# Optimization experiments

Measured on AMD Instinct MI355X. Metric: run time of the kernel, lower is better.

## Reference

```python
import jax, jax.numpy as jnp
import numpy as np

B, LQ, LKV, D, H = 4, 1024, 4096, 512, 4
HD = D // H  # head dim = 128


def setup_inputs() -> dict:
    key = jax.random.key(0)
    ks = jax.random.split(key, 6)
    s = 1.0 / np.sqrt(D)
    return {
        "x": jax.random.normal(ks[0], (B, LQ, D), jnp.float32),
        "encoder_feats": jax.random.normal(ks[1], (B, LKV, D), jnp.float32),
        "Wq": jax.random.normal(ks[2], (D, D), jnp.float32) * s,
        "Wk": jax.random.normal(ks[3], (D, D), jnp.float32) * s,
        "Wv": jax.random.normal(ks[4], (D, D), jnp.float32) * s,
        "bq": jnp.zeros((D,), jnp.float32),
        "bk": jnp.zeros((D,), jnp.float32),
        "bv": jnp.zeros((D,), jnp.float32),
        "Wo": jax.random.normal(ks[5], (D, D), jnp.float32) * s,
        "bo": jnp.zeros((D,), jnp.float32),
    }


def reference(x, encoder_feats, Wq, Wk, Wv, bq, bk, bv, Wo, bo):
    # nn.MultiheadAttention explicit (non-flash) path, dropout=0, eval.
    # Project, split heads: [B, L, D] -> [B, H, L, HD]
    def heads(t, L):
        return t.reshape(B, L, H, HD).transpose(0, 2, 1, 3)

    q = heads(x @ Wq.T + bq, LQ)
    k = heads(encoder_feats @ Wk.T + bk, LKV)
    v = heads(encoder_feats @ Wv.T + bv, LKV)

    scale = 1.0 / jnp.sqrt(jnp.asarray(HD, x.dtype))
    scores = jnp.einsum("bhqd,bhkd->bhqk", q, k) * scale  # [B,H,LQ,LKV]
    attn = jax.nn.softmax(scores, axis=-1)
    ctx = jnp.einsum("bhqk,bhkd->bhqd", attn, v)  # [B,H,LQ,HD]
    ctx = ctx.transpose(0, 2, 1, 3).reshape(B, LQ, D)
    attn_output = ctx @ Wo.T + bo
    # forward() returns attn_output only (fused/LayerNorm result is discarded)
    return attn_output
```

## Files before the change

kernel.cpp:

```cpp
#include <hip/hip_runtime.h>
#include <math.h>

#define B_    4
#define LQ_   1024
#define LKV_  4096
#define DM    512
#define NH    4
#define HD_   128

typedef _Float16 half8   __attribute__((ext_vector_type(8)));
typedef _Float16 half4_t __attribute__((ext_vector_type(4)));
typedef float    floatx4 __attribute__((ext_vector_type(4)));

#define MFMA16(a, b, c) __builtin_amdgcn_mfma_f32_16x16x32_f16((a), (b), (c), 0, 0, 0)

template<typename XT, int MODE>
__global__ __launch_bounds__(256) void proj_mfma(
    const XT* __restrict__ X,
    const float* __restrict__ W,
    const float* __restrict__ bias,
    void* __restrict__ Yv, float scale)
{
  __shared__ _Float16 SMEM[128 * 144];
  _Float16 (*Xs)[72] = (_Float16(*)[72])SMEM;
  _Float16 (*Ws)[72] = (_Float16(*)[72])(SMEM + 128 * 72);

  const int tid  = threadIdx.x;
  const int lane = tid & 63;
  const int w    = tid >> 6;
  const int n16  = lane & 15;
  const int quad = lane >> 4;
  const int wm   = (w & 1) * 64;
  const int wn   = (w >> 1) * 64;
  const int row0 = blockIdx.x * 128;
  const int col0 = blockIdx.y * 128;

  floatx4 acc[4][4];
#pragma unroll
  for (int a = 0; a < 4; ++a)
#pragma unroll
    for (int b = 0; b < 4; ++b) acc[a][b] = (floatx4){0.f, 0.f, 0.f, 0.f};

  for (int k0 = 0; k0 < 512; k0 += 64) {
#pragma unroll
    for (int i = 0; i < 4; ++i) {
      int c = i * 256 + tid;
      int r = c >> 3, off = (c & 7) * 8;
      half8 hx;
      if (sizeof(XT) == 4) {
        const float* xp = (const float*)X + (size_t)(row0 + r) * 512 + k0 + off;
        float4 a = *(const float4*)xp, b2 = *(const float4*)(xp + 4);
        hx[0] = (_Float16)a.x;  hx[1] = (_Float16)a.y;
        hx[2] = (_Float16)a.z;  hx[3] = (_Float16)a.w;
        hx[4] = (_Float16)b2.x; hx[5] = (_Float16)b2.y;
        hx[6] = (_Float16)b2.z; hx[7] = (_Float16)b2.w;
      } else {
        hx = *(const half8*)((const _Float16*)X + (size_t)(row0 + r) * 512 + k0 + off);
      }
      *(half8*)&Xs[r][off] = hx;
      const float* wp = W + (size_t)(col0 + r) * 512 + k0 + off;
      float4 wa = *(const float4*)wp, wb = *(const float4*)(wp + 4);
      half8 hw;
      hw[0] = (_Float16)wa.x; hw[1] = (_Float16)wa.y;
      hw[2] = (_Float16)wa.z; hw[3] = (_Float16)wa.w;
      hw[4] = (_Float16)wb.x; hw[5] = (_Float16)wb.y;
      hw[6] = (_Float16)wb.z; hw[7] = (_Float16)wb.w;
      *(half8*)&Ws[r][off] = hw;
    }
    __syncthreads();
#pragma unroll
    for (int kc = 0; kc < 2; ++kc) {
      half8 af[4], bf[4];
#pragma unroll
      for (int mb = 0; mb < 4; ++mb)
        af[mb] = *(const half8*)&Xs[wm + mb * 16 + n16][kc * 32 + quad * 8];
#pragma unroll
      for (int nb = 0; nb < 4; ++nb)
        bf[nb] = *(const half8*)&Ws[wn + nb * 16 + n16][kc * 32 + quad * 8];
#pragma unroll
      for (int mb = 0; mb < 4; ++mb)
#pragma unroll
        for (int nb = 0; nb < 4; ++nb)
          acc[mb][nb] = MFMA16(af[mb], bf[nb], acc[mb][nb]);
    }
    __syncthreads();
  }

  if (MODE == 2) {
    _Float16 (*Ts)[144] = (_Float16(*)[144])SMEM;
#pragma unroll
    for (int mb = 0; mb < 4; ++mb) {
#pragma unroll
      for (int nb = 0; nb < 4; ++nb) {
        int dl = wn + nb * 16 + n16;
        float bi = bias[col0 + dl];
        half4_t hv;
#pragma unroll
        for (int r = 0; r < 4; ++r) hv[r] = (_Float16)(acc[mb][nb][r] + bi);
        *(half4_t*)&Ts[dl][wm + mb * 16 + quad * 4] = hv;
      }
    }
    __syncthreads();
    int b   = row0 >> 12;
    int kv0 = row0 & 4095;
    _Float16* Vt = (_Float16*)Yv;
#pragma unroll
    for (int i = 0; i < 8; ++i) {
      int f = i * 256 + tid;
      int dl = f >> 4, kv8 = (f & 15) * 8;
      half8 ov = *(const half8*)&Ts[dl][kv8];
      *(half8*)(Vt + (size_t)((b * 4 + blockIdx.y) * 128 + dl) * LKV_ + kv0 + kv8) = ov;
    }
  } else {
#pragma unroll
    for (int mb = 0; mb < 4; ++mb) {
#pragma unroll
      for (int nb = 0; nb < 4; ++nb) {
#pragma unroll
        for (int r = 0; r < 4; ++r) {
          int row = row0 + wm + mb * 16 + quad * 4 + r;
          int col = col0 + wn + nb * 16 + n16;
          float v = (acc[mb][nb][r] + bias[col]) * scale;
          if (MODE == 0) ((float*)Yv)[(size_t)row * 512 + col] = v;
          else ((_Float16*)Yv)[(size_t)row * 512 + col] = (_Float16)v;
        }
      }
    }
  }
}

__global__ __launch_bounds__(256, 2) void flash_mfma2(
    const _Float16* __restrict__ Qh,
    const _Float16* __restrict__ Kh,
    const _Float16* __restrict__ Vtg,
    _Float16* __restrict__ Opart,
    float* __restrict__ ml)
{
  __shared__ _Float16 Ks[64][136];
  __shared__ _Float16 Vs[128][72];
  __shared__ _Float16 Ps[4][32][72];

  const int tid  = threadIdx.x;
  const int lane = tid & 63;
  const int w    = tid >> 6;
  const int n16  = lane & 15;
  const int quad = lane >> 4;

  const int xb    = blockIdx.x;
  const int qt    = blockIdx.y;
  const int split = xb & 3;
  const int bh    = xb >> 2;
  const int h = bh & 3, b = bh >> 2;

  const _Float16* Qg = Qh + (size_t)(b * LQ_ + qt * 128) * DM + h * HD_;
  const _Float16* Kg = Kh + (size_t)(b * LKV_) * DM + h * HD_;
  const _Float16* Vg = Vtg + (size_t)(bh * HD_) * LKV_;

  half8 qf[2][4];
  const int chunk = w >> 1;
  const int qrb   = (w & 1) * 32;
#pragma unroll
  for (int c = 0; c < 2; ++c) {
#pragma unroll
    for (int i = 0; i < 4; ++i) {
      int f = i * 256 + tid;
      int r = f >> 4, c8 = (f & 15) * 8;
      *(half8*)&Ks[r][c8] = *(const half8*)(Qg + (size_t)(c * 64 + r) * DM + c8);
    }
    __syncthreads();
    if (chunk == c) {
#pragma unroll
      for (int qb = 0; qb < 2; ++qb)
#pragma unroll
        for (int kc = 0; kc < 4; ++kc)
          qf[qb][kc] = *(const half8*)&Ks[qrb + qb * 16 + n16][kc * 32 + quad * 8];
    }
    __syncthreads();
  }

  floatx4 o[2][8];
#pragma unroll
  for (int mb = 0; mb < 2; ++mb)
#pragma unroll
    for (int vb = 0; vb < 8; ++vb) o[mb][vb] = (floatx4){0.f, 0.f, 0.f, 0.f};
  float m_i[2] = {-INFINITY, -INFINITY};
  float l_i[2] = {0.f, 0.f};

  for (int kt = split * 16; kt < split * 16 + 16; ++kt) {
#pragma unroll
    for (int i = 0; i < 4; ++i) {
      int f = i * 256 + tid;
      int r = f >> 4, c8 = (f & 15) * 8;
      *(half8*)&Ks[r][c8] = *(const half8*)(Kg + (size_t)(kt * 64 + r) * DM + c8);
    }
#pragma unroll
    for (int i = 0; i < 4; ++i) {
      int f = i * 256 + tid;
      int d = f >> 3, kv8 = (f & 7) * 8;
      *(half8*)&Vs[d][kv8] = *(const half8*)(Vg + (size_t)d * LKV_ + kt * 64 + kv8);
    }
    __syncthreads();

    floatx4 s[2][4];
#pragma unroll
    for (int qb = 0; qb < 2; ++qb)
#pragma unroll
      for (int cb = 0; cb < 4; ++cb) s[qb][cb] = (floatx4){0.f, 0.f, 0.f, 0.f};
#pragma unroll
    for (int cb = 0; cb < 4; ++cb) {
#pragma unroll
      for (int kc = 0; kc < 4; ++kc) {
        half8 kf = *(const half8*)&Ks[cb * 16 + n16][kc * 32 + quad * 8];
        s[0][cb] = MFMA16(kf, qf[0][kc], s[0][cb]);
        s[1][cb] = MFMA16(kf, qf[1][kc], s[1][cb]);
      }
    }

    float alpha[2];
#pragma unroll
    for (int qb = 0; qb < 2; ++qb) {
      float mx = -INFINITY;
#pragma unroll
      for (int cb = 0; cb < 4; ++cb)
#pragma unroll
        for (int r = 0; r < 4; ++r) mx = fmaxf(mx, s[qb][cb][r]);
      mx = fmaxf(mx, __shfl_xor(mx, 16));
      mx = fmaxf(mx, __shfl_xor(mx, 32));
      float mn = fmaxf(m_i[qb], mx);
      alpha[qb] = __expf(m_i[qb] - mn);
      m_i[qb] = mn;
      float rs = 0.f;
#pragma unroll
      for (int cb = 0; cb < 4; ++cb) {
        half4_t ph;
#pragma unroll
        for (int r = 0; r < 4; ++r) {
          float p = __expf(s[qb][cb][r] - mn);
          rs += p;
          ph[r] = (_Float16)p;
        }
        *(half4_t*)&Ps[w][qb * 16 + n16][cb * 16 + quad * 4] = ph;
      }
      rs += __shfl_xor(rs, 16);
      rs += __shfl_xor(rs, 32);
      l_i[qb] = l_i[qb] * alpha[qb] + rs;
    }

#pragma unroll
    for (int mb = 0; mb < 2; ++mb) {
#pragma unroll
      for (int r = 0; r < 4; ++r) {
        float a = __shfl(alpha[mb], (lane & 48) | (quad * 4 + r));
#pragma unroll
        for (int vb = 0; vb < 8; ++vb) o[mb][vb][r] *= a;
      }
    }

    half8 pf[2][2];
#pragma unroll
    for (int mb = 0; mb < 2; ++mb)
#pragma unroll
      for (int kc = 0; kc < 2; ++kc)
        pf[mb][kc] = *(const half8*)&Ps[w][mb * 16 + n16][kc * 32 + quad * 8];
#pragma unroll
    for (int vb = 0; vb < 8; ++vb) {
#pragma unroll
      for (int kc = 0; kc < 2; ++kc) {
        half8 vf = *(const half8*)&Vs[vb * 16 + n16][kc * 32 + quad * 8];
        o[0][vb] = MFMA16(pf[0][kc], vf, o[0][vb]);
        o[1][vb] = MFMA16(pf[1][kc], vf, o[1][vb]);
      }
    }
    __syncthreads();
  }

  _Float16* Og = Opart + ((size_t)xb * 1024 + qt * 128 + w * 32) * HD_;
#pragma unroll
  for (int mb = 0; mb < 2; ++mb) {
#pragma unroll
    for (int r = 0; r < 4; ++r) {
#pragma unroll
      for (int vb = 0; vb < 8; ++vb)
        Og[(size_t)(mb * 16 + quad * 4 + r) * HD_ + vb * 16 + n16] =
            (_Float16)o[mb][vb][r];
    }
  }
  if (quad == 0) {
#pragma unroll
    for (int qb = 0; qb < 2; ++qb) {
      size_t qi = (size_t)xb * 1024 + qt * 128 + w * 32 + qb * 16 + n16;
      ml[qi * 2] = m_i[qb];
      ml[qi * 2 + 1] = l_i[qb];
    }
  }
}

__global__ __launch_bounds__(256) void combine_splits(
    const _Float16* __restrict__ Opart,
    const float* __restrict__ ml,
    _Float16* __restrict__ CTXh)
{
  int g  = blockIdx.x * 2 + (threadIdx.x >> 7);
  int d  = threadIdx.x & 127;
  int bh = g >> 10, q = g & 1023;
  int b = bh >> 2, h = bh & 3;

  float m[4], l[4], M = -INFINITY;
#pragma unroll
  for (int p = 0; p < 4; ++p) {
    size_t idx = ((size_t)(bh * 4 + p) * 1024 + q) * 2;
    m[p] = ml[idx]; l[p] = ml[idx + 1];
    M = fmaxf(M, m[p]);
  }
  float L = 0.f, o = 0.f;
#pragma unroll
  for (int p = 0; p < 4; ++p) {
    float wgt = __expf(m[p] - M);
    L += wgt * l[p];
    o += wgt * (float)Opart[((size_t)(bh * 4 + p) * 1024 + q) * HD_ + d];
  }
  CTXh[(size_t)(b * LQ_ + q) * DM + h * HD_ + d] = (_Float16)(o / L);
}

extern "C" void kernel_launch(void* const* d_in, const int* in_sizes, int n_in,
                              void* d_out, int out_size, void* d_ws, size_t ws_size,
                              hipStream_t stream) {
  const float* x   = (const float*)d_in[0];
  const float* enc = (const float*)d_in[1];
  const float* Wq  = (const float*)d_in[2];
  const float* Wk  = (const float*)d_in[3];
  const float* Wv  = (const float*)d_in[4];
  const float* bq  = (const float*)d_in[5];
  const float* bk  = (const float*)d_in[6];
  const float* bv  = (const float*)d_in[7];
  const float* Wo  = (const float*)d_in[8];
  const float* bo  = (const float*)d_in[9];
  float* out = (float*)d_out;

  char* ws = (char*)d_ws;
  _Float16* Qh    = (_Float16*)(ws);
  _Float16* Kh    = (_Float16*)(ws + (4u  << 20));
  _Float16* Vtg   = (_Float16*)(ws + (20u << 20));
  _Float16* Opart = (_Float16*)(ws + (36u << 20));
  _Float16* CTXh  = (_Float16*)(ws + (52u << 20));
  float*    mlp   = (float*)   (ws + (56u << 20));

  const float qscale = 0.08838834764831845f;
  dim3 blk(256);

  proj_mfma<float, 1><<<dim3(32, 4),  blk, 0, stream>>>(x,   Wq, bq, Qh,  qscale);
  proj_mfma<float, 1><<<dim3(128, 4), blk, 0, stream>>>(enc, Wk, bk, Kh,  1.f);
  proj_mfma<float, 2><<<dim3(128, 4), blk, 0, stream>>>(enc, Wv, bv, Vtg, 1.f);

  flash_mfma2<<<dim3(64, 8), blk, 0, stream>>>(Qh, Kh, Vtg, Opart, mlp);

  combine_splits<<<dim3(8192), blk, 0, stream>>>(Opart, mlp, CTXh);

  proj_mfma<_Float16, 0><<<dim3(32, 4), blk, 0, stream>>>(CTXh, Wo, bo, out, 1.f);
}
```

Before: 229.6 us.

## Precast inputs to fp16, fuse K/V projection, and double flash KV splits

Adds a prep kernel that converts x, encoder features and all weights to fp16 once, so projections load half-precision directly. K and V projections are fused into one kernel sharing the encoder tile. The flash kernel uses 8 KV splits instead of 4, aliases the K and P shared buffers to raise occupancy to 4 blocks per CU, and the combine step merges 8 partials. This trades an extra cast pass and a larger partial-output buffer for less redundant conversion and better occupancy.

```diff
diff --git a/kernel.cpp b/kernel.cpp
--- a/kernel.cpp
+++ b/kernel.cpp
@@ -14,16 +14,40 @@
 
 #define MFMA16(a, b, c) __builtin_amdgcn_mfma_f32_16x16x32_f16((a), (b), (c), 0, 0, 0)
 
-template<typename XT, int MODE>
+__global__ __launch_bounds__(256) void prep_cast(
+    const float* __restrict__ x, const float* __restrict__ enc,
+    const float* __restrict__ Wq, const float* __restrict__ Wk,
+    const float* __restrict__ Wv, const float* __restrict__ Wo,
+    _Float16* __restrict__ xh, _Float16* __restrict__ ench,
+    _Float16* __restrict__ Wh)
+{
+  int i = blockIdx.x * 256 + threadIdx.x;
+  const float* src; _Float16* dst; size_t off;
+  if (i < 524288) { src = x; dst = xh; off = i; }
+  else if (i < 2621440) { src = enc; dst = ench; off = i - 524288; }
+  else {
+    int j = i - 2621440;
+    int wsel = j >> 16;
+    src = (wsel == 0) ? Wq : (wsel == 1) ? Wk : (wsel == 2) ? Wv : Wo;
+    dst = Wh + ((size_t)wsel << 18);
+    off = j & 65535;
+  }
+  float4 v = *(const float4*)(src + off * 4);
+  half4_t h;
+  h[0] = (_Float16)v.x; h[1] = (_Float16)v.y;
+  h[2] = (_Float16)v.z; h[3] = (_Float16)v.w;
+  *(half4_t*)(dst + off * 4) = h;
+}
+
+template<int MODE>
 __global__ __launch_bounds__(256) void proj_mfma(
-    const XT* __restrict__ X,
-    const float* __restrict__ W,
+    const _Float16* __restrict__ X,
+    const _Float16* __restrict__ W,
     const float* __restrict__ bias,
     void* __restrict__ Yv, float scale)
 {
-  __shared__ _Float16 SMEM[128 * 144];
-  _Float16 (*Xs)[72] = (_Float16(*)[72])SMEM;
-  _Float16 (*Ws)[72] = (_Float16(*)[72])(SMEM + 128 * 72);
+  __shared__ _Float16 Xs[128][72];
+  __shared__ _Float16 Ws[128][72];
 
   const int tid  = threadIdx.x;
   const int lane = tid & 63;
@@ -46,26 +70,8 @@
     for (int i = 0; i < 4; ++i) {
       int c = i * 256 + tid;
       int r = c >> 3, off = (c & 7) * 8;
-      half8 hx;
-      if (sizeof(XT) == 4) {
-        const float* xp = (const float*)X + (size_t)(row0 + r) * 512 + k0 + off;
-        float4 a = *(const float4*)xp, b2 = *(const float4*)(xp + 4);
-        hx[0] = (_Float16)a.x;  hx[1] = (_Float16)a.y;
-        hx[2] = (_Float16)a.z;  hx[3] = (_Float16)a.w;
-        hx[4] = (_Float16)b2.x; hx[5] = (_Float16)b2.y;
-        hx[6] = (_Float16)b2.z; hx[7] = (_Float16)b2.w;
-      } else {
-        hx = *(const half8*)((const _Float16*)X + (size_t)(row0 + r) * 512 + k0 + off);
-      }
-      *(half8*)&Xs[r][off] = hx;
-      const float* wp = W + (size_t)(col0 + r) * 512 + k0 + off;
-      float4 wa = *(const float4*)wp, wb = *(const float4*)(wp + 4);
-      half8 hw;
-      hw[0] = (_Float16)wa.x; hw[1] = (_Float16)wa.y;
-      hw[2] = (_Float16)wa.z; hw[3] = (_Float16)wa.w;
-      hw[4] = (_Float16)wb.x; hw[5] = (_Float16)wb.y;
-      hw[6] = (_Float16)wb.z; hw[7] = (_Float16)wb.w;
-      *(half8*)&Ws[r][off] = hw;
+      *(half8*)&Xs[r][off] = *(const half8*)(X + (size_t)(row0 + r) * 512 + k0 + off);
+      *(half8*)&Ws[r][off] = *(const half8*)(W + (size_t)(col0 + r) * 512 + k0 + off);
     }
     __syncthreads();
 #pragma unroll
@@ -86,59 +92,136 @@
     __syncthreads();
   }
 
-  if (MODE == 2) {
-    _Float16 (*Ts)[144] = (_Float16(*)[144])SMEM;
-#pragma unroll
-    for (int mb = 0; mb < 4; ++mb) {
+#pragma unroll
+  for (int mb = 0; mb < 4; ++mb) {
+#pragma unroll
+    for (int nb = 0; nb < 4; ++nb) {
+#pragma unroll
+      for (int r = 0; r < 4; ++r) {
+        int row = row0 + wm + mb * 16 + quad * 4 + r;
+        int col = col0 + wn + nb * 16 + n16;
+        float v = (acc[mb][nb][r] + bias[col]) * scale;
+        if (MODE == 0) ((float*)Yv)[(size_t)row * 512 + col] = v;
+        else ((_Float16*)Yv)[(size_t)row * 512 + col] = (_Float16)v;
+      }
+    }
+  }
+}
+
+__global__ __launch_bounds__(256, 2) void proj_kv(
+    const _Float16* __restrict__ Xe,
+    const _Float16* __restrict__ Wk,
+    const _Float16* __restrict__ Wv,
+    const float* __restrict__ bk,
+    const float* __restrict__ bv,
+    _Float16* __restrict__ Kh,
+    _Float16* __restrict__ Vt)
+{
+  __shared__ _Float16 SM[3 * 128 * 72];
+  _Float16 (*Xs)[72]  = (_Float16(*)[72])SM;
+  _Float16 (*Wks)[72] = (_Float16(*)[72])(SM + 128 * 72);
+  _Float16 (*Wvs)[72] = (_Float16(*)[72])(SM + 2 * 128 * 72);
+
+  const int tid  = threadIdx.x;
+  const int lane = tid & 63;
+  const int w    = tid >> 6;
+  const int n16  = lane & 15;
+  const int quad = lane >> 4;
+  const int wm   = (w & 1) * 64;
+  const int wn   = (w >> 1) * 64;
+  const int row0 = blockIdx.x * 128;
+  const int col0 = blockIdx.y * 128;
+
+  floatx4 accK[4][4], accV[4][4];
+#pragma unroll
+  for (int a = 0; a < 4; ++a)
+#pragma unroll
+    for (int b = 0; b < 4; ++b) {
+      accK[a][b] = (floatx4){0.f, 0.f, 0.f, 0.f};
+      accV[a][b] = (floatx4){0.f, 0.f, 0.f, 0.f};
+    }
+
+  for (int k0 = 0; k0 < 512; k0 += 64) {
+#pragma unroll
+    for (int i = 0; i < 4; ++i) {
+      int c = i * 256 + tid;
+      int r = c >> 3, off = (c & 7) * 8;
+      *(half8*)&Xs[r][off]  = *(const half8*)(Xe + (size_t)(row0 + r) * 512 + k0 + off);
+      *(half8*)&Wks[r][off] = *(const half8*)(Wk + (size_t)(col0 + r) * 512 + k0 + off);
+      *(half8*)&Wvs[r][off] = *(const half8*)(Wv + (size_t)(col0 + r) * 512 + k0 + off);
+    }
+    __syncthreads();
+#pragma unroll
+    for (int kc = 0; kc < 2; ++kc) {
+      half8 af[4], bkf[4], bvf[4];
+#pragma unroll
+      for (int mb = 0; mb < 4; ++mb)
+        af[mb] = *(const half8*)&Xs[wm + mb * 16 + n16][kc * 32 + quad * 8];
 #pragma unroll
       for (int nb = 0; nb < 4; ++nb) {
-        int dl = wn + nb * 16 + n16;
-        float bi = bias[col0 + dl];
-        half4_t hv;
-#pragma unroll
-        for (int r = 0; r < 4; ++r) hv[r] = (_Float16)(acc[mb][nb][r] + bi);
-        *(half4_t*)&Ts[dl][wm + mb * 16 + quad * 4] = hv;
-      }
-    }
-    __syncthreads();
-    int b   = row0 >> 12;
-    int kv0 = row0 & 4095;
-    _Float16* Vt = (_Float16*)Yv;
-#pragma unroll
-    for (int i = 0; i < 8; ++i) {
-      int f = i * 256 + tid;
-      int dl = f >> 4, kv8 = (f & 15) * 8;
-      half8 ov = *(const half8*)&Ts[dl][kv8];
-      *(half8*)(Vt + (size_t)((b * 4 + blockIdx.y) * 128 + dl) * LKV_ + kv0 + kv8) = ov;
-    }
-  } else {
-#pragma unroll
-    for (int mb = 0; mb < 4; ++mb) {
-#pragma unroll
-      for (int nb = 0; nb < 4; ++nb) {
-#pragma unroll
-        for (int r = 0; r < 4; ++r) {
-          int row = row0 + wm + mb * 16 + quad * 4 + r;
-          int col = col0 + wn + nb * 16 + n16;
-          float v = (acc[mb][nb][r] + bias[col]) * scale;
-          if (MODE == 0) ((float*)Yv)[(size_t)row * 512 + col] = v;
-          else ((_Float16*)Yv)[(size_t)row * 512 + col] = (_Float16)v;
+        bkf[nb] = *(const half8*)&Wks[wn + nb * 16 + n16][kc * 32 + quad * 8];
+        bvf[nb] = *(const half8*)&Wvs[wn + nb * 16 + n16][kc * 32 + quad * 8];
+      }
+#pragma unroll
+      for (int mb = 0; mb < 4; ++mb)
+#pragma unroll
+        for (int nb = 0; nb < 4; ++nb) {
+          accK[mb][nb] = MFMA16(af[mb], bkf[nb], accK[mb][nb]);
+          accV[mb][nb] = MFMA16(af[mb], bvf[nb], accV[mb][nb]);
         }
-      }
-    }
-  }
-}
-
-__global__ __launch_bounds__(256, 2) void flash_mfma2(
+    }
+    __syncthreads();
+  }
+
+#pragma unroll
+  for (int mb = 0; mb < 4; ++mb) {
+#pragma unroll
+    for (int nb = 0; nb < 4; ++nb) {
+#pragma unroll
+      for (int r = 0; r < 4; ++r) {
+        int row = row0 + wm + mb * 16 + quad * 4 + r;
+        int col = col0 + wn + nb * 16 + n16;
+        Kh[(size_t)row * 512 + col] = (_Float16)(accK[mb][nb][r] + bk[col]);
+      }
+    }
+  }
+
+  _Float16 (*Ts)[144] = (_Float16(*)[144])SM;
+#pragma unroll
+  for (int mb = 0; mb < 4; ++mb) {
+#pragma unroll
+    for (int nb = 0; nb < 4; ++nb) {
+      int dl = wn + nb * 16 + n16;
+      float bi = bv[col0 + dl];
+      half4_t hv;
+#pragma unroll
+      for (int r = 0; r < 4; ++r) hv[r] = (_Float16)(accV[mb][nb][r] + bi);
+      *(half4_t*)&Ts[dl][wm + mb * 16 + quad * 4] = hv;
+    }
+  }
+  __syncthreads();
+  int b   = row0 >> 12;
+  int kv0 = row0 & 4095;
+#pragma unroll
+  for (int i = 0; i < 8; ++i) {
+    int f = i * 256 + tid;
+    int dl = f >> 4, kv8 = (f & 15) * 8;
+    half8 ov = *(const half8*)&Ts[dl][kv8];
+    *(half8*)(Vt + (size_t)((b * 4 + blockIdx.y) * 128 + dl) * LKV_ + kv0 + kv8) = ov;
+  }
+}
+
+__global__ __launch_bounds__(256, 4) void flash_mfma2(
     const _Float16* __restrict__ Qh,
     const _Float16* __restrict__ Kh,
     const _Float16* __restrict__ Vtg,
     _Float16* __restrict__ Opart,
     float* __restrict__ ml)
 {
-  __shared__ _Float16 Ks[64][136];
+  __shared__ _Float16 U[4 * 32 * 72];
   __shared__ _Float16 Vs[128][72];
-  __shared__ _Float16 Ps[4][32][72];
+  _Float16 (*Ks)[136] = (_Float16(*)[136])U;
+  _Float16* Ps = U;
 
   const int tid  = threadIdx.x;
   const int lane = tid & 63;
@@ -148,8 +231,8 @@
 
   const int xb    = blockIdx.x;
   const int qt    = blockIdx.y;
-  const int split = xb & 3;
-  const int bh    = xb >> 2;
+  const int split = xb & 7;
+  const int bh    = xb >> 3;
   const int h = bh & 3, b = bh >> 2;
 
   const _Float16* Qg = Qh + (size_t)(b * LQ_ + qt * 128) * DM + h * HD_;
@@ -186,7 +269,7 @@
   float m_i[2] = {-INFINITY, -INFINITY};
   float l_i[2] = {0.f, 0.f};
 
-  for (int kt = split * 16; kt < split * 16 + 16; ++kt) {
+  for (int kt = split * 8; kt < split * 8 + 8; ++kt) {
 #pragma unroll
     for (int i = 0; i < 4; ++i) {
       int f = i * 256 + tid;
@@ -215,6 +298,7 @@
         s[1][cb] = MFMA16(kf, qf[1][kc], s[1][cb]);
       }
     }
+    __syncthreads();
 
     float alpha[2];
 #pragma unroll
@@ -239,7 +323,7 @@
           rs += p;
           ph[r] = (_Float16)p;
         }
-        *(half4_t*)&Ps[w][qb * 16 + n16][cb * 16 + quad * 4] = ph;
+        *(half4_t*)&Ps[(w * 32 + qb * 16 + n16) * 72 + cb * 16 + quad * 4] = ph;
       }
       rs += __shfl_xor(rs, 16);
       rs += __shfl_xor(rs, 32);
@@ -261,7 +345,7 @@
     for (int mb = 0; mb < 2; ++mb)
 #pragma unroll
       for (int kc = 0; kc < 2; ++kc)
-        pf[mb][kc] = *(const half8*)&Ps[w][mb * 16 + n16][kc * 32 + quad * 8];
+        pf[mb][kc] = *(const half8*)&Ps[(w * 32 + mb * 16 + n16) * 72 + kc * 32 + quad * 8];
 #pragma unroll
     for (int vb = 0; vb < 8; ++vb) {
 #pragma unroll
@@ -305,19 +389,19 @@
   int bh = g >> 10, q = g & 1023;
   int b = bh >> 2, h = bh & 3;
 
-  float m[4], l[4], M = -INFINITY;
-#pragma unroll
-  for (int p = 0; p < 4; ++p) {
-    size_t idx = ((size_t)(bh * 4 + p) * 1024 + q) * 2;
+  float m[8], l[8], M = -INFINITY;
+#pragma unroll
+  for (int p = 0; p < 8; ++p) {
+    size_t idx = ((size_t)(bh * 8 + p) * 1024 + q) * 2;
     m[p] = ml[idx]; l[p] = ml[idx + 1];
     M = fmaxf(M, m[p]);
   }
   float L = 0.f, o = 0.f;
 #pragma unroll
-  for (int p = 0; p < 4; ++p) {
+  for (int p = 0; p < 8; ++p) {
     float wgt = __expf(m[p] - M);
     L += wgt * l[p];
-    o += wgt * (float)Opart[((size_t)(bh * 4 + p) * 1024 + q) * HD_ + d];
+    o += wgt * (float)Opart[((size_t)(bh * 8 + p) * 1024 + q) * HD_ + d];
   }
   CTXh[(size_t)(b * LQ_ + q) * DM + h * HD_ + d] = (_Float16)(o / L);
 }
@@ -341,20 +425,29 @@
   _Float16* Qh    = (_Float16*)(ws);
   _Float16* Kh    = (_Float16*)(ws + (4u  << 20));
   _Float16* Vtg   = (_Float16*)(ws + (20u << 20));
+  _Float16* ench  = (_Float16*)(ws + (36u << 20));
+  _Float16* xh    = (_Float16*)(ws + (52u << 20));
   _Float16* Opart = (_Float16*)(ws + (36u << 20));
-  _Float16* CTXh  = (_Float16*)(ws + (52u << 20));
-  float*    mlp   = (float*)   (ws + (56u << 20));
+  _Float16* CTXh  = (_Float16*)(ws + (68u << 20));
+  float*    mlp   = (float*)   (ws + (72u << 20));
+  _Float16* Wh    = (_Float16*)(ws + (73u << 20));
+
+  _Float16* Whq = Wh;
+  _Float16* Whk = Wh + 262144;
+  _Float16* Whv = Wh + 524288;
+  _Float16* Who = Wh + 786432;
 
   const float qscale = 0.08838834764831845f;
   dim3 blk(256);
 
-  proj_mfma<float, 1><<<dim3(32, 4),  blk, 0, stream>>>(x,   Wq, bq, Qh,  qscale);
-  proj_mfma<float, 1><<<dim3(128, 4), blk, 0, stream>>>(enc, Wk, bk, Kh,  1.f);
-  proj_mfma<float, 2><<<dim3(128, 4), blk, 0, stream>>>(enc, Wv, bv, Vtg, 1.f);
-
-  flash_mfma2<<<dim3(64, 8), blk, 0, stream>>>(Qh, Kh, Vtg, Opart, mlp);
+  prep_cast<<<dim3(11264), blk, 0, stream>>>(x, enc, Wq, Wk, Wv, Wo, xh, ench, Wh);
+
+  proj_mfma<1><<<dim3(32, 4), blk, 0, stream>>>(xh, Whq, bq, Qh, qscale);
+  proj_kv<<<dim3(128, 4), blk, 0, stream>>>(ench, Whk, Whv, bk, bv, Kh, Vtg);
+
+  flash_mfma2<<<dim3(128, 8), blk, 0, stream>>>(Qh, Kh, Vtg, Opart, mlp);
 
   combine_splits<<<dim3(8192), blk, 0, stream>>>(Opart, mlp, CTXh);
 
-  proj_mfma<_Float16, 0><<<dim3(32, 4), blk, 0, stream>>>(CTXh, Wo, bo, out, 1.f);
-}
+  proj_mfma<0><<<dim3(32, 4), blk, 0, stream>>>(CTXh, Who, bo, out, 1.f);
+}
```

Measured after the change: 315.9 us. 1.38x slower.
